# Performance work log

Measured on AMD Instinct MI355X. Metric: run time of the kernel, lower is better.

The kernel has to match this reference:

```python
import jax, jax.numpy as jnp
import numpy as np

FACTOR = 5


def setup_inputs() -> dict:
    key = jax.random.key(0)
    k1, k2, k3 = jax.random.split(key, 3)
    B, L, H, E = 8, 3072, 8, 64
    return {
        "queries": jax.random.normal(k1, (B, L, H, E), dtype=jnp.float32),
        "keys": jax.random.normal(k2, (B, L, H, E), dtype=jnp.float32),
        "values": jax.random.normal(k3, (B, L, H, E), dtype=jnp.float32),
        "attn_mask": jnp.zeros((1,), dtype=jnp.int32),  # unused, matches torch signature
    }


def _autocorrelation(queries, keys, values):
    B, L, H, E = queries.shape
    # L == S here, so keys/values are used as-is (torch path: values[:, :L])
    qp = jnp.transpose(queries, (0, 2, 3, 1))  # [B,H,E,L]
    kp = jnp.transpose(keys, (0, 2, 3, 1))     # [B,H,E,L]
    vp = jnp.transpose(values, (0, 2, 3, 1))   # [B,H,D,L]

    # period-based dependencies via FFT cross-correlation
    q_fft = jnp.fft.rfft(qp, axis=-1)
    k_fft = jnp.fft.rfft(kp, axis=-1)
    corr = jnp.fft.irfft(q_fft * jnp.conj(k_fft), n=L, axis=-1)  # [B,H,E,L]

    # time-delay aggregation (training branch of the torch module)
    top_k = int(FACTOR * np.log(L))  # static (L known at trace time)
    mean_value = corr.mean(axis=1).mean(axis=1)            # [B,L]
    weights, index = jax.lax.top_k(mean_value, top_k)      # [B,K]
    tmp_corr = jax.nn.softmax(weights, axis=-1)            # [B,K]

    # torch uses only batch-0 shifts: roll(v, -index[0,i]) == gather (t + s) mod L
    shifts = index[0]                                      # [K]
    gather_idx = (jnp.arange(L)[None, :] + shifts[:, None]) % L  # [K,L]

    def step(acc, lag):
        idx_k, w_k = lag                    # idx_k: [L], w_k: [B]
        pattern = vp[..., idx_k]            # [B,H,D,L] rolled gather
        return acc + pattern * w_k[:, None, None, None], None

    agg, _ = jax.lax.scan(step, jnp.zeros_like(vp), (gather_idx, tmp_corr.T))
    return jnp.transpose(agg, (0, 3, 1, 2))  # [B,L,H,D]


def reference(queries, keys, values, attn_mask):
    return _autocorrelation(queries, keys, values)
```

## Files before the change

kernel.cpp:

```cpp
#include <hip/hip_runtime.h>
#include <math.h>

#define L_LEN  3072
#define CH512  512
#define TOPK   40
#define NBATCH 8
#define TWSZ   1088
#define SW(i)  ((i) + ((i) >> 5))
#define FFTSZ  3168

__device__ __forceinline__ void fft3072(float* re, float* im,
                                        const float* Ctab, const float* Stab,
                                        int tid, float sgn)
{
    #pragma unroll
    for (int s = 0; s < 10; s += 2) {
        int q = 1 << s;
        #pragma unroll
        for (int ii = 0; ii < 3; ii++) {
            int ib  = tid + (ii << 8);
            int sub = ib >> 8;
            int t   = ib & 255;
            int pos = t & (q - 1);
            int base= t >> s;
            int i0  = (sub << 10) + (base << (s + 2)) + pos;
            int p0 = SW(i0), p1 = SW(i0 + q), p2 = SW(i0 + 2*q), p3 = SW(i0 + 3*q);
            int j2 = 3 * (pos << (8 - s));
            int ph = j2 + (j2 >> 4);
            float c2 = Ctab[ph], s2 = sgn * Stab[ph];
            float c1 = c2*c2 - s2*s2, s1 = 2.0f*c2*s2;
            float a0r = re[p0], a0i = im[p0];
            float a1r = re[p1], a1i = im[p1];
            float a2r = re[p2], a2i = im[p2];
            float a3r = re[p3], a3i = im[p3];
            float t1r = c1*a1r - s1*a1i, t1i = c1*a1i + s1*a1r;
            float u0r = a0r + t1r, u0i = a0i + t1i;
            float u1r = a0r - t1r, u1i = a0i - t1i;
            float t3r = c1*a3r - s1*a3i, t3i = c1*a3i + s1*a3r;
            float u2r = a2r + t3r, u2i = a2i + t3i;
            float u3r = a2r - t3r, u3i = a2i - t3i;
            float w2r = c2*u2r - s2*u2i, w2i = c2*u2i + s2*u2r;
            float w3r = c2*u3r - s2*u3i, w3i = c2*u3i + s2*u3r;
            float iw3r = -sgn * w3i, iw3i = sgn * w3r;
            re[p0] = u0r + w2r;  im[p0] = u0i + w2i;
            re[p2] = u0r - w2r;  im[p2] = u0i - w2i;
            re[p1] = u1r + iw3r; im[p1] = u1i + iw3i;
            re[p3] = u1r - iw3r; im[p3] = u1i - iw3i;
        }
        __syncthreads();
    }
    #pragma unroll
    for (int ii = 0; ii < 4; ii++) {
        int kk = tid + (ii << 8);
        int ph = kk + (kk >> 4);
        float c1 = Ctab[ph];
        float s1 = sgn * Stab[ph];
        float c2 = c1*c1 - s1*s1;
        float s2 = 2.0f*c1*s1;
        int pk0 = SW(kk), pk1 = SW(1024 + kk), pk2 = SW(2048 + kk);
        float y0r = re[pk0], y0i = im[pk0];
        float y1r = re[pk1], y1i = im[pk1];
        float y2r = re[pk2], y2i = im[pk2];
        float t1r = c1*y1r - s1*y1i, t1i = c1*y1i + s1*y1r;
        float t2r = c2*y2r - s2*y2i, t2i = c2*y2i + s2*y2r;
        float ur = t1r + t2r, ui = t1i + t2i;
        float vr = t1r - t2r, vi = t1i - t2i;
        float mr = y0r - 0.5f*ur, mi = y0i - 0.5f*ui;
        float s3 = sgn * 0.86602540378443864676f;
        re[pk0] = y0r + ur;      im[pk0] = y0i + ui;
        re[pk1] = mr - s3*vi;    im[pk1] = mi + s3*vr;
        re[pk2] = mr + s3*vi;    im[pk2] = mi - s3*vr;
    }
    __syncthreads();
}

__device__ __forceinline__ void fill_twiddles(float* Ctab, float* Stab, int tid)
{
    const float TWO_PI = 6.28318530717958647692f;
    for (int j = tid; j < 1024; j += 256) {
        float ang = TWO_PI * (float)j / 3072.0f;
        float c, s;
        __sincosf(ang, &s, &c);
        int ph = j + (j >> 4);
        Ctab[ph] = c; Stab[ph] = s;
    }
}

__global__ __launch_bounds__(256) void transpose_kernel(
    const float* __restrict__ q, const float* __restrict__ k,
    float* __restrict__ qT, float* __restrict__ kT)
{
    __shared__ float tile[64][65];
    int which = blockIdx.z & 1;
    int b     = blockIdx.z >> 1;
    int l0    = blockIdx.x << 6;
    int c0    = blockIdx.y << 6;
    int x4 = threadIdx.x & 15;
    int y  = threadIdx.x >> 4;
    const float* src = which ? k : q;
    float* dst       = which ? kT : qT;
    size_t in_base = (size_t)b * L_LEN * CH512;
    #pragma unroll
    for (int p = 0; p < 4; p++) {
        int r = y + (p << 4);
        float4 v = *(const float4*)(src + in_base + (size_t)(l0 + r) * CH512 + c0 + (x4 << 2));
        tile[r][(x4 << 2) + 0] = v.x;
        tile[r][(x4 << 2) + 1] = v.y;
        tile[r][(x4 << 2) + 2] = v.z;
        tile[r][(x4 << 2) + 3] = v.w;
    }
    __syncthreads();
    size_t out_base = (size_t)b * CH512 * L_LEN;
    #pragma unroll
    for (int p = 0; p < 4; p++) {
        int c = y + (p << 4);
        float4 w;
        w.x = tile[(x4 << 2) + 0][c];
        w.y = tile[(x4 << 2) + 1][c];
        w.z = tile[(x4 << 2) + 2][c];
        w.w = tile[(x4 << 2) + 3][c];
        *(float4*)(dst + out_base + (size_t)(c0 + c) * L_LEN + l0 + (x4 << 2)) = w;
    }
}

__global__ __launch_bounds__(256, 4) void corr_fft_kernel(
    const float* __restrict__ qT, const float* __restrict__ kT,
    float* __restrict__ S_re, float* __restrict__ S_im)
{
    __shared__ float re[FFTSZ], im[FFTSZ];
    __shared__ float Ctab[TWSZ], Stab[TWSZ];
    int blk = blockIdx.x;
    int b   = blk >> 7;
    int c0  = (blk & 127) << 2;
    int tid = threadIdx.x;

    fill_twiddles(Ctab, Stab, tid);

    float accR[12], accI[12];
    #pragma unroll
    for (int it = 0; it < 12; it++) { accR[it] = 0.0f; accI[it] = 0.0f; }

    for (int ec = 0; ec < 4; ec++) {
        size_t ch_off = ((size_t)b * CH512 + c0 + ec) * L_LEN;
        const float4* q4 = (const float4*)(qT + ch_off);
        const float4* k4 = (const float4*)(kT + ch_off);
        __syncthreads();
        #pragma unroll
        for (int it = 0; it < 3; it++) {
            int idx = tid + (it << 8);
            float4 xq = q4[idx];
            float4 xk = k4[idx];
            #pragma unroll
            for (int j = 0; j < 4; j++) {
                int n = (idx << 2) + j;
                int m = n / 3;
                int r = n - 3 * m;
                int dst = SW((r << 10) + (__brev((unsigned)m) >> 22));
                float qv = (j == 0) ? xq.x : (j == 1) ? xq.y : (j == 2) ? xq.z : xq.w;
                float kv = (j == 0) ? xk.x : (j == 1) ? xk.y : (j == 2) ? xk.z : xk.w;
                re[dst] = qv;
                im[dst] = kv;
            }
        }
        __syncthreads();
        fft3072(re, im, Ctab, Stab, tid, -1.0f);
        #pragma unroll
        for (int it = 0; it < 12; it++) {
            int f = tid + (it << 8);
            int g = (f == 0) ? 0 : (L_LEN - f);
            int pf = SW(f), pg = SW(g);
            float ar = re[pf], ai = im[pf];
            float br = re[pg], bi = -im[pg];
            float ur = ar + br, ui = ai + bi;
            float vr = ar - br, vi = ai - bi;
            accR[it] += 0.25f * (ur * vi - ui * vr);
            accI[it] += 0.25f * (ur * vr + ui * vi);
        }
    }
    #pragma unroll
    for (int it = 0; it < 12; it++) {
        int f = tid + (it << 8);
        atomicAdd(&S_re[b * L_LEN + f], accR[it]);
        atomicAdd(&S_im[b * L_LEN + f], accI[it]);
    }
}

__global__ __launch_bounds__(256) void ifft_topk_kernel(
    const float* __restrict__ S_re, const float* __restrict__ S_im,
    float* __restrict__ wts, int* __restrict__ shifts)
{
    __shared__ float re[FFTSZ], im[FFTSZ];
    __shared__ float Ctab[TWSZ], Stab[TWSZ];
    __shared__ unsigned hist[256];
    __shared__ unsigned long long s_pref;
    __shared__ unsigned s_need;
    __shared__ unsigned s_cnt;
    __shared__ unsigned selk[TOPK];
    __shared__ unsigned selidx[TOPK];
    __shared__ float sv[TOPK];
    __shared__ int   si[TOPK];

    int b = blockIdx.x;
    int tid = threadIdx.x;
    fill_twiddles(Ctab, Stab, tid);
    #pragma unroll
    for (int it = 0; it < 12; it++) {
        int n = tid + (it << 8);
        int m = n / 3;
        int r = n - 3 * m;
        int dst = SW((r << 10) + (__brev((unsigned)m) >> 22));
        re[dst] = S_re[b * L_LEN + n];
        im[dst] = S_im[b * L_LEN + n];
    }
    __syncthreads();
    fft3072(re, im, Ctab, Stab, tid, 1.0f);

    unsigned* key = (unsigned*)im;
    const float scale = 1.0f / (3072.0f * 512.0f);
    #pragma unroll
    for (int it = 0; it < 12; it++) {
        int t = tid + (it << 8);
        float v = re[SW(t)] * scale;
        unsigned u = __float_as_uint(v);
        key[t] = (u & 0x80000000u) ? ~u : (u | 0x80000000u);
    }
    if (tid == 0) { s_pref = 0ULL; s_need = TOPK; s_cnt = 0u; }
    __syncthreads();

    #pragma unroll
    for (int p = 5; p >= 0; --p) {
        hist[tid] = 0u;
        __syncthreads();
        unsigned long long pref = s_pref;
        unsigned need = s_need;
        #pragma unroll
        for (int it = 0; it < 12; it++) {
            int t = tid + (it << 8);
            unsigned long long c = ((unsigned long long)key[t] << 12) | (unsigned)(4095 - t);
            if ((c >> ((p + 1) * 8)) == (pref >> ((p + 1) * 8)))
                atomicAdd(&hist[(unsigned)((c >> (p * 8)) & 0xFFu)], 1u);
        }
        __syncthreads();
        if (tid < 64) {
            int l = tid;
            unsigned s0 = hist[4*l] + hist[4*l+1] + hist[4*l+2] + hist[4*l+3];
            unsigned T = s0;
            #pragma unroll
            for (int off = 1; off < 64; off <<= 1) {
                unsigned o = __shfl_down(T, off);
                if (l + off < 64) T += o;
            }
            unsigned above = T - s0;
            if (T >= need && above < need) {
                unsigned acc = above;
                int bin = -1;
                #pragma unroll
                for (int j = 3; j >= 0; --j) {
                    unsigned h = hist[4*l + j];
                    if (bin < 0) {
                        if (acc + h >= need) bin = 4*l + j;
                        else acc += h;
                    }
                }
                s_pref = pref | ((unsigned long long)(unsigned)bin << (p * 8));
                s_need = need - acc;
            }
        }
        __syncthreads();
    }

    unsigned long long cstar = s_pref;
    #pragma unroll
    for (int it = 0; it < 12; it++) {
        int t = tid + (it << 8);
        unsigned long long c = ((unsigned long long)key[t] << 12) | (unsigned)(4095 - t);
        if (c >= cstar) {
            unsigned pos = atomicAdd(&s_cnt, 1u);
            if (pos < TOPK) { selk[pos] = key[t]; selidx[pos] = (unsigned)t; }
        }
    }
    __syncthreads();

    if (tid < TOPK) {
        unsigned mk = selk[tid], mi = selidx[tid];
        unsigned long long mc = ((unsigned long long)mk << 12) | (unsigned)(4095 - mi);
        int rank = 0;
        #pragma unroll
        for (int j = 0; j < TOPK; j++) {
            unsigned long long cj = ((unsigned long long)selk[j] << 12) | (unsigned)(4095 - selidx[j]);
            rank += (cj > mc) ? 1 : 0;
        }
        unsigned u = (mk & 0x80000000u) ? (mk ^ 0x80000000u) : ~mk;
        sv[rank] = __uint_as_float(u);
        si[rank] = (int)mi;
    }
    __syncthreads();

    if (tid == 0) {
        float mx = sv[0];
        float sum = 0.0f;
        float ex[TOPK];
        for (int kk = 0; kk < TOPK; kk++) { ex[kk] = __expf(sv[kk] - mx); sum += ex[kk]; }
        float inv = 1.0f / sum;
        for (int kk = 0; kk < TOPK; kk++) wts[b * TOPK + kk] = ex[kk] * inv;
        if (b == 0)
            for (int kk = 0; kk < TOPK; kk++) shifts[kk] = si[kk];
    }
}

__global__ __launch_bounds__(256) void agg_kernel(
    const float* __restrict__ v, const float* __restrict__ wts,
    const int* __restrict__ shifts, float* __restrict__ out)
{
    __shared__ float w[TOPK];
    __shared__ int   sh[TOPK];
    int idx  = blockIdx.x;
    int slab = idx & 7;
    int rest = idx >> 3;
    int tile = rest % 192;
    int b    = rest / 192;
    int tid  = threadIdx.x;
    if (tid < TOPK) { w[tid] = wts[b * TOPK + tid]; sh[tid] = shifts[tid]; }
    __syncthreads();
    int t  = (tile << 4) + (tid >> 4);
    int ch = (slab << 6) + ((tid & 15) << 2);
    size_t vbase = (size_t)b * L_LEN * CH512;
    float4 acc = make_float4(0.0f, 0.0f, 0.0f, 0.0f);
    #pragma unroll 8
    for (int kk = 0; kk < TOPK; kk++) {
        int tt = t + sh[kk];
        if (tt >= L_LEN) tt -= L_LEN;
        const float4 x = *(const float4*)(v + vbase + (size_t)tt * CH512 + ch);
        float ww = w[kk];
        acc.x += x.x * ww; acc.y += x.y * ww;
        acc.z += x.z * ww; acc.w += x.w * ww;
    }
    *(float4*)(out + vbase + (size_t)t * CH512 + ch) = acc;
}

extern "C" void kernel_launch(void* const* d_in, const int* in_sizes, int n_in,
                              void* d_out, int out_size, void* d_ws, size_t ws_size,
                              hipStream_t stream)
{
    const float* q = (const float*)d_in[0];
    const float* k = (const float*)d_in[1];
    const float* v = (const float*)d_in[2];
    float* out = (float*)d_out;
    float* ws  = (float*)d_ws;

    const size_t TSZ = (size_t)NBATCH * CH512 * L_LEN;

    float* qT = out;
    float* kT = ws;
    float* S_re = ws + TSZ;
    float* S_im = S_re + NBATCH * L_LEN;
    float* wts  = S_im + NBATCH * L_LEN;
    int*   shifts = (int*)(wts + NBATCH * TOPK);

    hipMemsetAsync(S_re, 0, (size_t)2 * NBATCH * L_LEN * sizeof(float), stream);

    transpose_kernel<<<dim3(L_LEN / 64, CH512 / 64, NBATCH * 2), dim3(256), 0, stream>>>(
        q, k, qT, kT);
    corr_fft_kernel<<<dim3(1024), dim3(256), 0, stream>>>(qT, kT, S_re, S_im);
    ifft_topk_kernel<<<dim3(NBATCH), dim3(256), 0, stream>>>(S_re, S_im, wts, shifts);
    agg_kernel<<<dim3(8 * (L_LEN / 16) * NBATCH), dim3(256), 0, stream>>>(v, wts, shifts, out);
}
```

Measured before the change: 343.1 us.

## Stage value columns in LDS and gather shifted lags from shared memory

The aggregation kernel now assigns each block one batch and one 4-channel column, loads the full 3072-long column into LDS once, and computes all 40 shifted weighted sums from LDS with six outputs per thread. This removes the repeated global/L2 gathers of the value tensor for every lag. In exchange, the global loads are strided by a full row, using only 16 bytes per 2KB stride, and each block uses 48KB of LDS, which limits occupancy.

```diff
diff --git a/kernel.cpp b/kernel.cpp
--- a/kernel.cpp
+++ b/kernel.cpp
@@ -308,34 +308,53 @@
     }
 }
 
-__global__ __launch_bounds__(256) void agg_kernel(
+__global__ __launch_bounds__(512) void agg_kernel(
     const float* __restrict__ v, const float* __restrict__ wts,
     const int* __restrict__ shifts, float* __restrict__ out)
 {
+    __shared__ float4 vcol[L_LEN];
     __shared__ float w[TOPK];
     __shared__ int   sh[TOPK];
-    int idx  = blockIdx.x;
-    int slab = idx & 7;
-    int rest = idx >> 3;
-    int tile = rest % 192;
-    int b    = rest / 192;
-    int tid  = threadIdx.x;
+    int idx = blockIdx.x;
+    int cg  = idx & 127;
+    int b   = idx >> 7;
+    int tid = threadIdx.x;
+    int ch  = cg << 2;
     if (tid < TOPK) { w[tid] = wts[b * TOPK + tid]; sh[tid] = shifts[tid]; }
-    __syncthreads();
-    int t  = (tile << 4) + (tid >> 4);
-    int ch = (slab << 6) + ((tid & 15) << 2);
-    size_t vbase = (size_t)b * L_LEN * CH512;
-    float4 acc = make_float4(0.0f, 0.0f, 0.0f, 0.0f);
+    size_t vbase = (size_t)b * L_LEN * CH512 + ch;
+    #pragma unroll
+    for (int it = 0; it < 6; it++) {
+        int r = tid + (it << 9);
+        vcol[r] = *(const float4*)(v + vbase + (size_t)r * CH512);
+    }
+    __syncthreads();
+    float4 acc0 = make_float4(0.f,0.f,0.f,0.f);
+    float4 acc1 = acc0, acc2 = acc0, acc3 = acc0, acc4 = acc0, acc5 = acc0;
     #pragma unroll 8
     for (int kk = 0; kk < TOPK; kk++) {
-        int tt = t + sh[kk];
-        if (tt >= L_LEN) tt -= L_LEN;
-        const float4 x = *(const float4*)(v + vbase + (size_t)tt * CH512 + ch);
         float ww = w[kk];
-        acc.x += x.x * ww; acc.y += x.y * ww;
-        acc.z += x.z * ww; acc.w += x.w * ww;
-    }
-    *(float4*)(out + vbase + (size_t)t * CH512 + ch) = acc;
+        int s = sh[kk];
+        int t0 = tid + s;            if (t0 >= L_LEN) t0 -= L_LEN;
+        int t1 = tid + 512 + s;      if (t1 >= L_LEN) t1 -= L_LEN;
+        int t2 = tid + 1024 + s;     if (t2 >= L_LEN) t2 -= L_LEN;
+        int t3 = tid + 1536 + s;     if (t3 >= L_LEN) t3 -= L_LEN;
+        int t4 = tid + 2048 + s;     if (t4 >= L_LEN) t4 -= L_LEN;
+        int t5 = tid + 2560 + s;     if (t5 >= L_LEN) t5 -= L_LEN;
+        float4 x0 = vcol[t0], x1 = vcol[t1], x2 = vcol[t2];
+        float4 x3 = vcol[t3], x4 = vcol[t4], x5 = vcol[t5];
+        acc0.x += x0.x*ww; acc0.y += x0.y*ww; acc0.z += x0.z*ww; acc0.w += x0.w*ww;
+        acc1.x += x1.x*ww; acc1.y += x1.y*ww; acc1.z += x1.z*ww; acc1.w += x1.w*ww;
+        acc2.x += x2.x*ww; acc2.y += x2.y*ww; acc2.z += x2.z*ww; acc2.w += x2.w*ww;
+        acc3.x += x3.x*ww; acc3.y += x3.y*ww; acc3.z += x3.z*ww; acc3.w += x3.w*ww;
+        acc4.x += x4.x*ww; acc4.y += x4.y*ww; acc4.z += x4.z*ww; acc4.w += x4.w*ww;
+        acc5.x += x5.x*ww; acc5.y += x5.y*ww; acc5.z += x5.z*ww; acc5.w += x5.w*ww;
+    }
+    *(float4*)(out + vbase + (size_t)(tid         ) * CH512) = acc0;
+    *(float4*)(out + vbase + (size_t)(tid + 512   ) * CH512) = acc1;
+    *(float4*)(out + vbase + (size_t)(tid + 1024  ) * CH512) = acc2;
+    *(float4*)(out + vbase + (size_t)(tid + 1536  ) * CH512) = acc3;
+    *(float4*)(out + vbase + (size_t)(tid + 2048  ) * CH512) = acc4;
+    *(float4*)(out + vbase + (size_t)(tid + 2560  ) * CH512) = acc5;
 }
 
 extern "C" void kernel_launch(void* const* d_in, const int* in_sizes, int n_in,
@@ -363,5 +382,5 @@
         q, k, qT, kT);
     corr_fft_kernel<<<dim3(1024), dim3(256), 0, stream>>>(qT, kT, S_re, S_im);
     ifft_topk_kernel<<<dim3(NBATCH), dim3(256), 0, stream>>>(S_re, S_im, wts, shifts);
-    agg_kernel<<<dim3(8 * (L_LEN / 16) * NBATCH), dim3(256), 0, stream>>>(v, wts, shifts, out);
-}
+    agg_kernel<<<dim3(NBATCH * (CH512 / 4)), dim3(512), 0, stream>>>(v, wts, shifts, out);
+}
```

New measurement: 364.5 us. 6.2% more time.
